# Optimization experiments

Measured on AMD Instinct MI355X. Metric: run time of the kernel, lower is better.

Reference implementation:

```python
import jax, jax.numpy as jnp
import numpy as np

N, E, CIN, COUT, KHOP = 100000, 600000, 128, 128, 3


def setup_inputs() -> dict:
    key = jax.random.key(0)
    k1, k2, k3 = jax.random.split(key, 3)
    x = jax.random.normal(k1, (N, CIN), dtype=jnp.float32)
    edge_index = jax.random.randint(k2, (2, E), 0, N, dtype=jnp.int64)
    # xavier_uniform init for weight [in, out]
    limit = float(np.sqrt(6.0 / (CIN + COUT)))
    weight = jax.random.uniform(k3, (CIN, COUT), minval=-limit, maxval=limit, dtype=jnp.float32)
    bias = jnp.zeros((COUT,), jnp.float32)
    log_scale = jnp.asarray(np.log(1.0), jnp.float32)  # init_scale = 1.0
    hop_logits = jnp.zeros((KHOP + 1,), jnp.float32)
    return {"x": x, "edge_index": edge_index, "num_nodes": N,
            "weight": weight, "bias": bias,
            "log_scale": log_scale, "hop_logits": hop_logits}


def reference(x, edge_index, num_nodes, weight, bias, log_scale, hop_logits):
    src, dst = edge_index[0], edge_index[1]
    # symmetric normalization D_src^{-1/2} A D_dst^{-1/2}, no self-loops
    ones = jnp.ones(src.shape, x.dtype)
    deg_src = jax.ops.segment_sum(ones, src, num_segments=num_nodes)
    deg_dst = jax.ops.segment_sum(ones, dst, num_segments=num_nodes)
    dsi = jnp.where(deg_src > 0, jax.lax.rsqrt(jnp.maximum(deg_src, 1.0)), 0.0)
    ddi = jnp.where(deg_dst > 0, jax.lax.rsqrt(jnp.maximum(deg_dst, 1.0)), 0.0)
    edge_weight = dsi[src] * ddi[dst]  # [E]

    s = jnp.exp(log_scale)
    alpha = jax.nn.softmax(hop_logits)  # [k_hop+1]

    wavelet_out = alpha[0] * x
    current = x
    for k in range(1, KHOP + 1):  # small fixed hop count
        # A_hat @ current : gather -> scale -> scatter-add
        current = jax.ops.segment_sum(current[src] * edge_weight[:, None], dst,
                                      num_segments=num_nodes)
        decay = jnp.exp(-s * k)
        wavelet_out = wavelet_out + alpha[k] * decay * current

    return wavelet_out @ weight + bias
```

## Files before the change

kernel.cpp:

```cpp
#include <hip/hip_runtime.h>
#include <hip/hip_bf16.h>

#define C 128

typedef short s16x8 __attribute__((ext_vector_type(8)));
typedef float f32x4 __attribute__((ext_vector_type(4)));
typedef float f32x2 __attribute__((ext_vector_type(2)));

static __device__ __forceinline__ float b2f(unsigned short u) {
    union { unsigned int i; float f; } v;
    v.i = ((unsigned int)u) << 16;
    return v.f;
}
static __device__ __forceinline__ unsigned short f2b(float f) {
    __hip_bfloat16 b = __float2bfloat16(f);
    return *reinterpret_cast<unsigned short*>(&b);
}

__global__ __launch_bounds__(256) void zero_int_kernel(int4* __restrict__ p, long n4) {
    long i = blockIdx.x * 256L + threadIdx.x;
    if (i < n4) p[i] = make_int4(0, 0, 0, 0);
}

__global__ __launch_bounds__(256) void hist_kernel(
    const int* __restrict__ ei, int E,
    int* __restrict__ degs, int* __restrict__ degd) {
    int i = blockIdx.x * 256 + threadIdx.x;
    int e0 = i * 4;
    if (e0 + 4 <= E) {
        int4 s = *(const int4*)(ei + e0);
        int4 d = *(const int4*)(ei + E + e0);
        atomicAdd(&degs[s.x], 1); atomicAdd(&degs[s.y], 1);
        atomicAdd(&degs[s.z], 1); atomicAdd(&degs[s.w], 1);
        atomicAdd(&degd[d.x], 1); atomicAdd(&degd[d.y], 1);
        atomicAdd(&degd[d.z], 1); atomicAdd(&degd[d.w], 1);
    } else {
        for (int e = e0; e < E; ++e) {
            atomicAdd(&degs[ei[e]], 1);
            atomicAdd(&degd[ei[E + e]], 1);
        }
    }
}

__global__ __launch_bounds__(256) void rpscan_kernel(const int* __restrict__ degd,
                                                     int* __restrict__ rp,
                                                     int* __restrict__ cursor,
                                                     int* __restrict__ gctr, int N) {
    __shared__ int sm[256];
    __shared__ int base_sm;
    int t = threadIdx.x;
    int i = blockIdx.x * 256 + t;
    int v = (i < N) ? degd[i] : 0;
    sm[t] = v;
    __syncthreads();
    for (int off = 1; off < 256; off <<= 1) {
        int add = (t >= off) ? sm[t - off] : 0;
        __syncthreads();
        sm[t] += add;
        __syncthreads();
    }
    if (t == 255) base_sm = atomicAdd(gctr, sm[255]);
    __syncthreads();
    if (i < N) {
        int r = base_sm + sm[t] - v;
        rp[i] = r;
        cursor[i] = r;
    }
}

__global__ __launch_bounds__(256) void conv8wt_kernel(
    const float* __restrict__ x, const int* __restrict__ degs,
    unsigned int* __restrict__ x8g, long n4,
    const float* __restrict__ W, unsigned short* __restrict__ WtB,
    const float* __restrict__ log_scale, const float* __restrict__ hop_logits,
    float* __restrict__ coef, int convBlocks) {
    if ((int)blockIdx.x >= convBlocks) {
        int tid = ((int)blockIdx.x - convBlocks) * 256 + threadIdx.x;
        int k = tid & 127, c = tid >> 7;
        WtB[c * 128 + k] = f2b(W[k * 128 + c]);
        if (tid == 0) {
            float s = expf(log_scale[0]);
            float m = hop_logits[0];
            for (int kk = 1; kk < 4; ++kk) m = fmaxf(m, hop_logits[kk]);
            float a[4], sum = 0.0f;
            for (int kk = 0; kk < 4; ++kk) { a[kk] = expf(hop_logits[kk] - m); sum += a[kk]; }
            for (int kk = 0; kk < 4; ++kk) coef[kk] = (a[kk] / sum) * expf(-s * (float)kk);
        }
        return;
    }
    long i = blockIdx.x * 256L + threadIdx.x;
    if (i >= n4) return;
    int n = (int)(i >> 5);
    int od = degs[n];
    float w = od > 0 ? rsqrtf((float)od) : 0.0f;
    float4 v = ((const float4*)x)[i];
    int r = __builtin_amdgcn_cvt_pk_fp8_f32(w * v.x, w * v.y, 0, false);
    r = __builtin_amdgcn_cvt_pk_fp8_f32(w * v.z, w * v.w, r, true);
    x8g[i] = (unsigned int)r;
}

__global__ __launch_bounds__(256) void scatter_kernel(const int* __restrict__ ei, int E,
                                                      int* __restrict__ cursor,
                                                      unsigned int* __restrict__ csrp) {
    int i = blockIdx.x * 256 + threadIdx.x;
    int e0 = i * 4;
    if (e0 + 4 <= E) {
        int4 s = *(const int4*)(ei + e0);
        int4 d = *(const int4*)(ei + E + e0);
        int p0 = atomicAdd(&cursor[d.x], 1);
        int p1 = atomicAdd(&cursor[d.y], 1);
        int p2 = atomicAdd(&cursor[d.z], 1);
        int p3 = atomicAdd(&cursor[d.w], 1);
        csrp[p0] = (unsigned int)s.x;
        csrp[p1] = (unsigned int)s.y;
        csrp[p2] = (unsigned int)s.z;
        csrp[p3] = (unsigned int)s.w;
    } else {
        for (int e = e0; e < E; ++e) {
            int s = ei[e];
            int d = ei[E + e];
            int pos = atomicAdd(&cursor[d], 1);
            csrp[pos] = (unsigned int)s;
        }
    }
}

__global__ __launch_bounds__(256) void pullg_kernel(
    const int* __restrict__ rp, const int* __restrict__ degd,
    const int* __restrict__ degs,
    const unsigned int* __restrict__ csrp,
    const unsigned short* __restrict__ src_g,
    unsigned short* __restrict__ h8, unsigned short* __restrict__ g8, int N) {
    int wid = (int)((blockIdx.x * 256L + threadIdx.x) >> 6);
    if (wid >= N) return;
    int lane = threadIdx.x & 63;
    int beg = __builtin_amdgcn_readfirstlane(rp[wid]);
    int cnt = __builtin_amdgcn_readfirstlane(degd[wid]);
    float sx = 0.f, sy = 0.f;
    if (cnt > 0) {
        for (int j = 0; j < cnt; j += 8) {
            int   idx[8];
            float mk[8];
            #pragma unroll
            for (int i = 0; i < 8; ++i) {
                int jj = j + i;
                bool ok = jj < cnt;
                idx[i] = (int)csrp[beg + (ok ? jj : 0)];
                mk[i] = ok ? 1.0f : 0.0f;
            }
            unsigned short u[8];
            #pragma unroll
            for (int i = 0; i < 8; ++i) u[i] = src_g[(long)idx[i] * 64 + lane];
            #pragma unroll
            for (int i = 0; i < 8; ++i) {
                f32x2 v = __builtin_amdgcn_cvt_pk_f32_fp8((int)u[i], false);
                sx += mk[i] * v[0];
                sy += mk[i] * v[1];
            }
        }
        float dv = rsqrtf((float)cnt);
        sx *= dv; sy *= dv;
    }
    int od = __builtin_amdgcn_readfirstlane(degs[wid]);
    float ds = od > 0 ? rsqrtf((float)od) : 0.0f;
    long rb = (long)wid * 64 + lane;
    h8[rb] = (unsigned short)__builtin_amdgcn_cvt_pk_fp8_f32(sx, sy, 0, false);
    g8[rb] = (unsigned short)__builtin_amdgcn_cvt_pk_fp8_f32(ds * sx, ds * sy, 0, false);
}

__global__ __launch_bounds__(256) void pull3c8_kernel(
    const int* __restrict__ rp, const int* __restrict__ degd,
    const unsigned int* __restrict__ csrp,
    const unsigned short* __restrict__ g2_8,
    const float* __restrict__ x,
    const unsigned short* __restrict__ h1_8,
    const unsigned short* __restrict__ h2_8,
    const float* __restrict__ coef,
    unsigned int* __restrict__ hc, int N) {
    int wid = (int)((blockIdx.x * 256L + threadIdx.x) >> 6);
    if (wid >= N) return;
    int lane = threadIdx.x & 63;
    int beg = __builtin_amdgcn_readfirstlane(rp[wid]);
    int cnt = __builtin_amdgcn_readfirstlane(degd[wid]);
    float sx = 0.f, sy = 0.f;
    if (cnt > 0) {
        for (int j = 0; j < cnt; j += 8) {
            int   idx[8];
            float mk[8];
            #pragma unroll
            for (int i = 0; i < 8; ++i) {
                int jj = j + i;
                bool ok = jj < cnt;
                idx[i] = (int)csrp[beg + (ok ? jj : 0)];
                mk[i] = ok ? 1.0f : 0.0f;
            }
            unsigned short u[8];
            #pragma unroll
            for (int i = 0; i < 8; ++i) u[i] = g2_8[(long)idx[i] * 64 + lane];
            #pragma unroll
            for (int i = 0; i < 8; ++i) {
                f32x2 v = __builtin_amdgcn_cvt_pk_f32_fp8((int)u[i], false);
                sx += mk[i] * v[0];
                sy += mk[i] * v[1];
            }
        }
        float dv = rsqrtf((float)cnt);
        sx *= dv; sy *= dv;
    }
    float c0 = coef[0], c1 = coef[1], c2 = coef[2], c3 = coef[3];
    long rb = (long)wid * 64 + lane;
    float2 xv = *(const float2*)(x + (long)wid * C + lane * 2);
    f32x2 v1 = __builtin_amdgcn_cvt_pk_f32_fp8((int)h1_8[rb], false);
    f32x2 v2 = __builtin_amdgcn_cvt_pk_f32_fp8((int)h2_8[rb], false);
    float f0 = c0 * xv.x + c1 * v1[0] + c2 * v2[0] + c3 * sx;
    float f1 = c0 * xv.y + c1 * v1[1] + c2 * v2[1] + c3 * sy;
    hc[rb] = (unsigned int)f2b(f0) | ((unsigned int)f2b(f1) << 16);
}

__global__ __launch_bounds__(256) void gemm_kernel(
    const unsigned short* __restrict__ hc,
    const unsigned short* __restrict__ WtB,
    const float* __restrict__ bias,
    float* __restrict__ out, int N) {
    __shared__ unsigned short Wl[128 * 136];
    int t = threadIdx.x;

    #pragma unroll
    for (int i = 0; i < 8; ++i) {
        int ch = t + i * 256;
        int r = ch >> 4;
        int ko = (ch & 15) * 8;
        *(s16x8*)(Wl + r * 136 + ko) = *(const s16x8*)(WtB + r * 128 + ko);
    }
    __syncthreads();

    int wave = t >> 6, lane = t & 63;
    int lsel = lane & 15;
    int lk   = (lane >> 4) * 8;
    int arow = blockIdx.x * 64 + wave * 16 + lsel;
    bool rok = arow < N;
    long rbase = (long)arow * C;

    f32x4 acc[8];
    #pragma unroll
    for (int i = 0; i < 8; ++i) acc[i] = (f32x4){0.f, 0.f, 0.f, 0.f};

    #pragma unroll
    for (int ks = 0; ks < 4; ++ks) {
        int k0 = ks * 32 + lk;
        s16x8 a = rok ? *(const s16x8*)(hc + rbase + k0) : (s16x8)0;
        #pragma unroll
        for (int cf = 0; cf < 8; ++cf) {
            s16x8 b = *(const s16x8*)(Wl + (cf * 16 + lsel) * 136 + k0);
            acc[cf] = __builtin_amdgcn_mfma_f32_16x16x32_bf16(a, b, acc[cf], 0, 0, 0);
        }
    }

    int orow0 = blockIdx.x * 64 + wave * 16 + (lane >> 4) * 4;
    #pragma unroll
    for (int cf = 0; cf < 8; ++cf) {
        int ocol = cf * 16 + lsel;
        float bv = bias[ocol];
        #pragma unroll
        for (int r = 0; r < 4; ++r) {
            int orow = orow0 + r;
            if (orow < N) out[(long)orow * C + ocol] = acc[cf][r] + bv;
        }
    }
}

extern "C" void kernel_launch(void* const* d_in, const int* in_sizes, int n_in,
                              void* d_out, int out_size, void* d_ws, size_t ws_size,
                              hipStream_t stream) {
    const float* x          = (const float*)d_in[0];
    const int*   ei         = (const int*)d_in[1];
    const float* W          = (const float*)d_in[3];
    const float* bias       = (const float*)d_in[4];
    const float* log_scale  = (const float*)d_in[5];
    const float* hop_logits = (const float*)d_in[6];
    float* out = (float*)d_out;

    int N = in_sizes[0] / C;
    int E = in_sizes[1] / 2;

    char* ws = (char*)d_ws;
    size_t f8b = (size_t)N * C;
    unsigned short* x8g = (unsigned short*)ws;
    unsigned short* g1  = (unsigned short*)(ws + f8b);
    unsigned short* h1  = (unsigned short*)(ws + 2 * f8b);
    unsigned short* g2  = (unsigned short*)(ws + 3 * f8b);
    unsigned short* h2  = (unsigned short*)(ws + 4 * f8b);
    unsigned short* hc  = (unsigned short*)(ws + 5 * f8b);
    unsigned int* csrp  = (unsigned int*)(ws + 7 * f8b);
    int*   degs    = (int*)(csrp + E);
    int*   degd    = degs + N;
    int*   gctr    = degd + N;
    int*   rp      = gctr + 16;
    int*   cursor  = rp + N;
    float* coef    = (float*)(cursor + N);
    unsigned short* WtB = (unsigned short*)(coef + 4);

    int eb4 = (E / 4 + 255) / 256 + 1;
    int nbk = (N + 255) / 256;
    int pull_blocks = (int)(((long)N * 64 + 255) / 256);
    long n4 = (long)N * C / 4;
    int convBlocks = (int)((n4 + 255) / 256);

    long zn4 = (2L * N + 16 + 3) / 4;
    zero_int_kernel<<<(int)((zn4 + 255) / 256), 256, 0, stream>>>((int4*)degs, zn4);
    hist_kernel<<<eb4, 256, 0, stream>>>(ei, E, degs, degd);
    rpscan_kernel<<<nbk, 256, 0, stream>>>(degd, rp, cursor, gctr, N);
    conv8wt_kernel<<<convBlocks + 64, 256, 0, stream>>>(x, degs, (unsigned int*)x8g, n4,
                                                        W, WtB, log_scale, hop_logits,
                                                        coef, convBlocks);
    scatter_kernel<<<eb4, 256, 0, stream>>>(ei, E, cursor, csrp);

    pullg_kernel<<<pull_blocks, 256, 0, stream>>>(rp, degd, degs, csrp, x8g, h1, g1, N);
    pullg_kernel<<<pull_blocks, 256, 0, stream>>>(rp, degd, degs, csrp, g1,  h2, g2, N);

    pull3c8_kernel<<<pull_blocks, 256, 0, stream>>>(rp, degd, csrp, g2, x, h1, h2, coef,
                                                    (unsigned int*)hc, N);

    gemm_kernel<<<(N + 63) / 64, 256, 0, stream>>>(hc, WtB, bias, out, N);
}
```

Baseline: 227.8 us.

## Drop per-hop h buffers, rebuild them from g via sqrt(deg), merge scan and convert kernels

The hop kernels now store only the source-degree-scaled fp8 features g and no longer write a separate unscaled copy h. The final combine kernel rebuilds h1 and h2 by multiplying g1 and g2 by sqrt(out-degree); zero-degree nodes use a scale of 1 so nothing is lost. This removes two full N×128 fp8 writes and shrinks the workspace. The row-pointer scan, the fp8 input conversion and the weight transpose are folded into a single launch, saving one kernel launch. The degree histogram now handles one edge per thread instead of four. The rescaling adds an extra fp8 rounding path, which slightly changes the accuracy of the h terms.

```diff
diff --git a/kernel.cpp b/kernel.cpp
--- a/kernel.cpp
+++ b/kernel.cpp
@@ -7,11 +7,6 @@
 typedef float f32x4 __attribute__((ext_vector_type(4)));
 typedef float f32x2 __attribute__((ext_vector_type(2)));
 
-static __device__ __forceinline__ float b2f(unsigned short u) {
-    union { unsigned int i; float f; } v;
-    v.i = ((unsigned int)u) << 16;
-    return v.f;
-}
 static __device__ __forceinline__ unsigned short f2b(float f) {
     __hip_bfloat16 b = __float2bfloat16(f);
     return *reinterpret_cast<unsigned short*>(&b);
@@ -25,78 +20,68 @@
 __global__ __launch_bounds__(256) void hist_kernel(
     const int* __restrict__ ei, int E,
     int* __restrict__ degs, int* __restrict__ degd) {
-    int i = blockIdx.x * 256 + threadIdx.x;
-    int e0 = i * 4;
-    if (e0 + 4 <= E) {
-        int4 s = *(const int4*)(ei + e0);
-        int4 d = *(const int4*)(ei + E + e0);
-        atomicAdd(&degs[s.x], 1); atomicAdd(&degs[s.y], 1);
-        atomicAdd(&degs[s.z], 1); atomicAdd(&degs[s.w], 1);
-        atomicAdd(&degd[d.x], 1); atomicAdd(&degd[d.y], 1);
-        atomicAdd(&degd[d.z], 1); atomicAdd(&degd[d.w], 1);
-    } else {
-        for (int e = e0; e < E; ++e) {
-            atomicAdd(&degs[ei[e]], 1);
-            atomicAdd(&degd[ei[E + e]], 1);
-        }
-    }
-}
-
-__global__ __launch_bounds__(256) void rpscan_kernel(const int* __restrict__ degd,
-                                                     int* __restrict__ rp,
-                                                     int* __restrict__ cursor,
-                                                     int* __restrict__ gctr, int N) {
-    __shared__ int sm[256];
-    __shared__ int base_sm;
-    int t = threadIdx.x;
-    int i = blockIdx.x * 256 + t;
-    int v = (i < N) ? degd[i] : 0;
-    sm[t] = v;
-    __syncthreads();
-    for (int off = 1; off < 256; off <<= 1) {
-        int add = (t >= off) ? sm[t - off] : 0;
-        __syncthreads();
-        sm[t] += add;
-        __syncthreads();
-    }
-    if (t == 255) base_sm = atomicAdd(gctr, sm[255]);
-    __syncthreads();
-    if (i < N) {
-        int r = base_sm + sm[t] - v;
-        rp[i] = r;
-        cursor[i] = r;
-    }
-}
-
-__global__ __launch_bounds__(256) void conv8wt_kernel(
+    int e = blockIdx.x * 256 + threadIdx.x;
+    if (e < E) {
+        atomicAdd(&degs[ei[e]], 1);
+        atomicAdd(&degd[ei[E + e]], 1);
+    }
+}
+
+__global__ __launch_bounds__(256) void rcw_kernel(
+    const int* __restrict__ degd, int* __restrict__ rp,
+    int* __restrict__ cursor, int* __restrict__ gctr, int N, int nbk,
     const float* __restrict__ x, const int* __restrict__ degs,
-    unsigned int* __restrict__ x8g, long n4,
+    unsigned int* __restrict__ x8g, long n4, int convBlocks,
     const float* __restrict__ W, unsigned short* __restrict__ WtB,
     const float* __restrict__ log_scale, const float* __restrict__ hop_logits,
-    float* __restrict__ coef, int convBlocks) {
-    if ((int)blockIdx.x >= convBlocks) {
-        int tid = ((int)blockIdx.x - convBlocks) * 256 + threadIdx.x;
-        int k = tid & 127, c = tid >> 7;
-        WtB[c * 128 + k] = f2b(W[k * 128 + c]);
-        if (tid == 0) {
-            float s = expf(log_scale[0]);
-            float m = hop_logits[0];
-            for (int kk = 1; kk < 4; ++kk) m = fmaxf(m, hop_logits[kk]);
-            float a[4], sum = 0.0f;
-            for (int kk = 0; kk < 4; ++kk) { a[kk] = expf(hop_logits[kk] - m); sum += a[kk]; }
-            for (int kk = 0; kk < 4; ++kk) coef[kk] = (a[kk] / sum) * expf(-s * (float)kk);
+    float* __restrict__ coef) {
+    int b = (int)blockIdx.x;
+    if (b < nbk) {
+        __shared__ int sm[256];
+        __shared__ int base_sm;
+        int t = threadIdx.x;
+        int i = b * 256 + t;
+        int v = (i < N) ? degd[i] : 0;
+        sm[t] = v;
+        __syncthreads();
+        for (int off = 1; off < 256; off <<= 1) {
+            int add = (t >= off) ? sm[t - off] : 0;
+            __syncthreads();
+            sm[t] += add;
+            __syncthreads();
+        }
+        if (t == 255) base_sm = atomicAdd(gctr, sm[255]);
+        __syncthreads();
+        if (i < N) {
+            int r = base_sm + sm[t] - v;
+            rp[i] = r;
+            cursor[i] = r;
         }
         return;
     }
-    long i = blockIdx.x * 256L + threadIdx.x;
-    if (i >= n4) return;
-    int n = (int)(i >> 5);
-    int od = degs[n];
-    float w = od > 0 ? rsqrtf((float)od) : 0.0f;
-    float4 v = ((const float4*)x)[i];
-    int r = __builtin_amdgcn_cvt_pk_fp8_f32(w * v.x, w * v.y, 0, false);
-    r = __builtin_amdgcn_cvt_pk_fp8_f32(w * v.z, w * v.w, r, true);
-    x8g[i] = (unsigned int)r;
+    if (b < nbk + convBlocks) {
+        long i = (long)(b - nbk) * 256 + threadIdx.x;
+        if (i >= n4) return;
+        int n = (int)(i >> 5);
+        int od = degs[n];
+        float w = od > 0 ? rsqrtf((float)od) : 1.0f;
+        float4 v = ((const float4*)x)[i];
+        int r = __builtin_amdgcn_cvt_pk_fp8_f32(w * v.x, w * v.y, 0, false);
+        r = __builtin_amdgcn_cvt_pk_fp8_f32(w * v.z, w * v.w, r, true);
+        x8g[i] = (unsigned int)r;
+        return;
+    }
+    int tid = (b - nbk - convBlocks) * 256 + threadIdx.x;
+    int k = tid & 127, c = tid >> 7;
+    WtB[c * 128 + k] = f2b(W[k * 128 + c]);
+    if (tid == 0) {
+        float s = expf(log_scale[0]);
+        float m = hop_logits[0];
+        for (int kk = 1; kk < 4; ++kk) m = fmaxf(m, hop_logits[kk]);
+        float a[4], sum = 0.0f;
+        for (int kk = 0; kk < 4; ++kk) { a[kk] = expf(hop_logits[kk] - m); sum += a[kk]; }
+        for (int kk = 0; kk < 4; ++kk) coef[kk] = (a[kk] / sum) * expf(-s * (float)kk);
+    }
 }
 
 __global__ __launch_bounds__(256) void scatter_kernel(const int* __restrict__ ei, int E,
@@ -130,7 +115,7 @@
     const int* __restrict__ degs,
     const unsigned int* __restrict__ csrp,
     const unsigned short* __restrict__ src_g,
-    unsigned short* __restrict__ h8, unsigned short* __restrict__ g8, int N) {
+    unsigned short* __restrict__ g8, int N) {
     int wid = (int)((blockIdx.x * 256L + threadIdx.x) >> 6);
     if (wid >= N) return;
     int lane = threadIdx.x & 63;
@@ -162,19 +147,18 @@
         sx *= dv; sy *= dv;
     }
     int od = __builtin_amdgcn_readfirstlane(degs[wid]);
-    float ds = od > 0 ? rsqrtf((float)od) : 0.0f;
-    long rb = (long)wid * 64 + lane;
-    h8[rb] = (unsigned short)__builtin_amdgcn_cvt_pk_fp8_f32(sx, sy, 0, false);
-    g8[rb] = (unsigned short)__builtin_amdgcn_cvt_pk_fp8_f32(ds * sx, ds * sy, 0, false);
+    float ds = od > 0 ? rsqrtf((float)od) : 1.0f;
+    g8[(long)wid * 64 + lane] =
+        (unsigned short)__builtin_amdgcn_cvt_pk_fp8_f32(ds * sx, ds * sy, 0, false);
 }
 
 __global__ __launch_bounds__(256) void pull3c8_kernel(
     const int* __restrict__ rp, const int* __restrict__ degd,
+    const int* __restrict__ degs,
     const unsigned int* __restrict__ csrp,
     const unsigned short* __restrict__ g2_8,
     const float* __restrict__ x,
-    const unsigned short* __restrict__ h1_8,
-    const unsigned short* __restrict__ h2_8,
+    const unsigned short* __restrict__ g1_8,
     const float* __restrict__ coef,
     unsigned int* __restrict__ hc, int N) {
     int wid = (int)((blockIdx.x * 256L + threadIdx.x) >> 6);
@@ -207,13 +191,15 @@
         float dv = rsqrtf((float)cnt);
         sx *= dv; sy *= dv;
     }
+    int od = __builtin_amdgcn_readfirstlane(degs[wid]);
+    float inv = od > 0 ? sqrtf((float)od) : 1.0f;
     float c0 = coef[0], c1 = coef[1], c2 = coef[2], c3 = coef[3];
     long rb = (long)wid * 64 + lane;
     float2 xv = *(const float2*)(x + (long)wid * C + lane * 2);
-    f32x2 v1 = __builtin_amdgcn_cvt_pk_f32_fp8((int)h1_8[rb], false);
-    f32x2 v2 = __builtin_amdgcn_cvt_pk_f32_fp8((int)h2_8[rb], false);
-    float f0 = c0 * xv.x + c1 * v1[0] + c2 * v2[0] + c3 * sx;
-    float f1 = c0 * xv.y + c1 * v1[1] + c2 * v2[1] + c3 * sy;
+    f32x2 v1 = __builtin_amdgcn_cvt_pk_f32_fp8((int)g1_8[rb], false);
+    f32x2 v2 = __builtin_amdgcn_cvt_pk_f32_fp8((int)g2_8[rb], false);
+    float f0 = c0 * xv.x + c1 * v1[0] * inv + c2 * v2[0] * inv + c3 * sx;
+    float f1 = c0 * xv.y + c1 * v1[1] * inv + c2 * v2[1] * inv + c3 * sy;
     hc[rb] = (unsigned int)f2b(f0) | ((unsigned int)f2b(f1) << 16);
 }
 
@@ -287,11 +273,9 @@
     size_t f8b = (size_t)N * C;
     unsigned short* x8g = (unsigned short*)ws;
     unsigned short* g1  = (unsigned short*)(ws + f8b);
-    unsigned short* h1  = (unsigned short*)(ws + 2 * f8b);
-    unsigned short* g2  = (unsigned short*)(ws + 3 * f8b);
-    unsigned short* h2  = (unsigned short*)(ws + 4 * f8b);
-    unsigned short* hc  = (unsigned short*)(ws + 5 * f8b);
-    unsigned int* csrp  = (unsigned int*)(ws + 7 * f8b);
+    unsigned short* g2  = (unsigned short*)(ws + 2 * f8b);
+    unsigned short* hc  = (unsigned short*)(ws + 3 * f8b);
+    unsigned int* csrp  = (unsigned int*)(ws + 5 * f8b);
     int*   degs    = (int*)(csrp + E);
     int*   degd    = degs + N;
     int*   gctr    = degd + N;
@@ -300,6 +284,7 @@
     float* coef    = (float*)(cursor + N);
     unsigned short* WtB = (unsigned short*)(coef + 4);
 
+    int eb1 = (E + 255) / 256;
     int eb4 = (E / 4 + 255) / 256 + 1;
     int nbk = (N + 255) / 256;
     int pull_blocks = (int)(((long)N * 64 + 255) / 256);
@@ -308,17 +293,17 @@
 
     long zn4 = (2L * N + 16 + 3) / 4;
     zero_int_kernel<<<(int)((zn4 + 255) / 256), 256, 0, stream>>>((int4*)degs, zn4);
-    hist_kernel<<<eb4, 256, 0, stream>>>(ei, E, degs, degd);
-    rpscan_kernel<<<nbk, 256, 0, stream>>>(degd, rp, cursor, gctr, N);
-    conv8wt_kernel<<<convBlocks + 64, 256, 0, stream>>>(x, degs, (unsigned int*)x8g, n4,
-                                                        W, WtB, log_scale, hop_logits,
-                                                        coef, convBlocks);
+    hist_kernel<<<eb1, 256, 0, stream>>>(ei, E, degs, degd);
+    rcw_kernel<<<nbk + convBlocks + 64, 256, 0, stream>>>(
+        degd, rp, cursor, gctr, N, nbk,
+        x, degs, (unsigned int*)x8g, n4, convBlocks,
+        W, WtB, log_scale, hop_logits, coef);
     scatter_kernel<<<eb4, 256, 0, stream>>>(ei, E, cursor, csrp);
 
-    pullg_kernel<<<pull_blocks, 256, 0, stream>>>(rp, degd, degs, csrp, x8g, h1, g1, N);
-    pullg_kernel<<<pull_blocks, 256, 0, stream>>>(rp, degd, degs, csrp, g1,  h2, g2, N);
-
-    pull3c8_kernel<<<pull_blocks, 256, 0, stream>>>(rp, degd, csrp, g2, x, h1, h2, coef,
+    pullg_kernel<<<pull_blocks, 256, 0, stream>>>(rp, degd, degs, csrp, x8g, g1, N);
+    pullg_kernel<<<pull_blocks, 256, 0, stream>>>(rp, degd, degs, csrp, g1,  g2, N);
+
+    pull3c8_kernel<<<pull_blocks, 256, 0, stream>>>(rp, degd, degs, csrp, g2, x, g1, coef,
                                                     (unsigned int*)hc, N);
 
     gemm_kernel<<<(N + 63) / 64, 256, 0, stream>>>(hc, WtB, bias, out, N);
```

After: 224.5 us. About the same (-1.4%).
